# Kernel optimization log

Measured on AMD Instinct MI355X. Metric: run time of the kernel, lower is better.

Reference implementation:

```python
import jax, jax.numpy as jnp
import numpy as np

KS = 5          # kernel_size
D = 2           # spatial dim
DX = 0.01       # region kernel spacing
SCALE = 1.0
NX, NY = 32, 32
N = NX * NY


def _region_kernel():
    # gaussians.region_kernel: KS x KS grid of offsets spaced DX, centered at 0
    off = (jnp.arange(KS, dtype=jnp.float32) - (KS - 1) / 2.0) * DX
    gx, gy = jnp.meshgrid(off, off, indexing='ij')
    return jnp.stack([gx, gy], -1).reshape(-1, D)  # (KS*KS, 2)


def _build_cov(scaling, transform):
    # Cholesky-style parameterization: L lower-triangular with diag=scaling,
    # off-diag=transform; cov = L @ L^T (d=2 closed form)
    s0, s1 = scaling[:, 0], scaling[:, 1]
    t = transform[:, 0]
    c00 = s0 * s0
    c01 = s0 * t
    c11 = t * t + s1 * s1
    return jnp.stack([jnp.stack([c00, c01], -1), jnp.stack([c01, c11], -1)], -2)


def _inv2x2(c):
    det = c[:, 0, 0] * c[:, 1, 1] - c[:, 0, 1] * c[:, 1, 0]
    inv = jnp.stack([jnp.stack([c[:, 1, 1], -c[:, 0, 1]], -1),
                     jnp.stack([-c[:, 1, 0], c[:, 0, 0]], -1)], -2)
    return inv / det[:, None, None]


def setup_inputs() -> dict:
    key = jax.random.key(0)
    ks = jax.random.split(key, 20)
    # Gaussian state: grid means as in __init__
    tx = jnp.linspace(-1.0, 1.0, NX) * SCALE
    ty = jnp.linspace(-1.0, 1.0, NY) * SCALE
    gx, gy = jnp.meshgrid(tx, ty, indexing='ij')
    means = jnp.stack([gx, gy], -1).reshape(-1, D).astype(jnp.float32)
    u = 0.1 * jax.random.normal(ks[0], (N, 1), jnp.float32)
    scaling = jnp.exp(-4.5 + 0.2 * jax.random.normal(ks[1], (N, D), jnp.float32)) * SCALE
    transform = 0.002 * jax.random.normal(ks[2], (N, 1), jnp.float32)
    opacities = 2.0 + 0.1 * jax.random.normal(ks[3], (N,), jnp.float32)
    # network weights (4 heads share the first 3 layer shapes)
    convW = 0.05 * jax.random.normal(ks[4], (4, 50, 3, KS, KS), jnp.float32)
    convb = 0.01 * jax.random.normal(ks[5], (4, 50), jnp.float32)
    embW = 0.3 * jax.random.normal(ks[6], (4, 7, 30), jnp.float32)
    embb = 0.01 * jax.random.normal(ks[7], (4, 30), jnp.float32)
    l1W = 0.1 * jax.random.normal(ks[8], (4, 80, 80), jnp.float32)
    l1b = 0.01 * jax.random.normal(ks[9], (4, 80), jnp.float32)
    outW_sol = 0.1 * jax.random.normal(ks[10], (80, 1), jnp.float32)
    outb_sol = 0.01 * jax.random.normal(ks[11], (1,), jnp.float32)
    outW_trans = 0.1 * jax.random.normal(ks[12], (80, 2), jnp.float32)
    outb_trans = 0.01 * jax.random.normal(ks[13], (2,), jnp.float32)
    outW_scale = 0.1 * jax.random.normal(ks[14], (80, 2), jnp.float32)
    outb_scale = 0.01 * jax.random.normal(ks[15], (2,), jnp.float32)
    outW_tform = 0.1 * jax.random.normal(ks[16], (80, 1), jnp.float32)
    outb_tform = 0.01 * jax.random.normal(ks[17], (1,), jnp.float32)
    return {"means": means, "u": u, "scaling": scaling, "transform": transform,
            "opacities": opacities, "convW": convW, "convb": convb,
            "embW": embW, "embb": embb, "l1W": l1W, "l1b": l1b,
            "outW_sol": outW_sol, "outb_sol": outb_sol,
            "outW_trans": outW_trans, "outb_trans": outb_trans,
            "outW_scale": outW_scale, "outb_scale": outb_scale,
            "outW_tform": outW_tform, "outb_tform": outb_tform}


def reference(means, u, scaling, transform, opacities, convW, convb, embW, embb,
              l1W, l1b, outW_sol, outb_sol, outW_trans, outb_trans,
              outW_scale, outb_scale, outW_tform, outb_tform):
    n = means.shape[0]
    cov = _build_cov(scaling, transform)          # (N,2,2)
    conics = _inv2x2(cov)                         # (N,2,2)

    # --- sampling (torch.no_grad block in original) ---
    kern = _region_kernel()                                        # (25,2)
    samples = (means[:, None, :] + kern[None]).reshape(-1, D)      # (M,2), M=N*25
    bc = jnp.all(jnp.abs(samples) < SCALE, -1).astype(means.dtype)[:, None]
    alpha = jax.nn.sigmoid(opacities)                              # (N,)
    diff = samples[:, None, :] - means[None, :, :]                 # (M,N,2)
    Cq = jnp.einsum('nij,mnj->mni', conics, diff)                  # (M,N,2)
    G = jnp.exp(-0.5 * jnp.einsum('mni,mni->mn', diff, Cq)) * alpha[None, :]  # (M,N)
    u_s = G @ u                                                    # (M,1)
    # DIFFUSION pde_rhs = trace of laplacian: sum_n G * (|C q|^2 - tr(C)) * u_n
    trC = conics[:, 0, 0] + conics[:, 1, 1]
    lap = jnp.einsum('mn,mn,nc->mc', G, (Cq ** 2).sum(-1) - trC[None, :], u)  # (M,1)
    in_samples = jax.lax.stop_gradient(jnp.concatenate([u_s, lap, bc], -1))   # (M,3)

    # (N, 25, 3) -> (N, 3, 5, 5)
    img = in_samples.reshape(n, KS * KS, -1).transpose(0, 2, 1).reshape(n, -1, KS, KS)
    in_params = jnp.concatenate([means, u, scaling, transform, opacities[:, None]], -1)  # (N,7)

    # 4 Networks: conv(5x5 -> 1x1, 50ch) + param embed(7->30) + MLP(80->80->out)
    y = jnp.tanh(jnp.einsum('ncij,kocij->kno', img, convW) + convb[:, None, :])   # (4,N,50)
    e = jnp.tanh(jnp.einsum('nf,kfg->kng', in_params, embW) + embb[:, None, :])   # (4,N,30)
    h = jnp.tanh(jnp.einsum('knf,kfg->kng', jnp.concatenate([y, e], -1), l1W)
                 + l1b[:, None, :])                                               # (4,N,80)

    deltas = h[0] @ outW_sol + outb_sol          # (N,1)
    translation = h[1] @ outW_trans + outb_trans # (N,2)
    dscale = h[2] @ outW_scale + outb_scale      # (N,2)
    dtransform = h[3] @ outW_tform + outb_tform  # (N,1)

    u_new = u + deltas
    means_new = means + translation
    scaling_new = scaling * jnp.exp(dscale)
    transform_new = transform + dtransform
    cov_new = _build_cov(scaling_new, transform_new)
    return (u_new, means_new, scaling_new, transform_new, cov_new)
```

## Files before the change

### kernel.cpp

```cpp
#include <hip/hip_runtime.h>
#include <hip/hip_bf16.h>


#define NG 1024
#define GCAP 320

__device__ __forceinline__ float tanh_fast(float x) {
    return 1.0f - 2.0f / (__expf(2.0f * x) + 1.0f);
}

__global__ __launch_bounds__(256) void k_fused(
    const float* __restrict__ means, const float* __restrict__ u,
    const float* __restrict__ scal, const float* __restrict__ trans,
    const float* __restrict__ opac,
    const float* __restrict__ convW, const float* __restrict__ convb,
    const float* __restrict__ embW,  const float* __restrict__ embb,
    const float* __restrict__ l1W,   const float* __restrict__ l1b,
    const float* __restrict__ oWs,  const float* __restrict__ obs,
    const float* __restrict__ oWt,  const float* __restrict__ obt,
    const float* __restrict__ oWsc, const float* __restrict__ obsc,
    const float* __restrict__ oWtf, const float* __restrict__ obtf,
    float* __restrict__ out)
{
    __shared__ float gcomp[GCAP * 8];
    __shared__ float s1w[64 * 80];
    __shared__ float pus[2][2][32];
    __shared__ float plap[2][2][32];
    __shared__ float simg[2][80];
    __shared__ float hin[2][4][80];
    __shared__ float hv[2][4][80];
    __shared__ float semb[840];
    __shared__ float sembb[120];
    __shared__ float shead[480];
    __shared__ float sheadb[6];
    __shared__ int   cnt;

    const int t  = threadIdx.x;
    const int n0 = blockIdx.x * 2;

    const float mx0 = means[2*n0],   my0 = means[2*n0+1];
    const float mx1 = means[2*n0+2], my1 = means[2*n0+3];
    const float uu0 = u[n0],     uu1 = u[n0+1];
    const float sc00 = scal[2*n0],   sc01 = scal[2*n0+1];
    const float sc10 = scal[2*n0+2], sc11 = scal[2*n0+3];
    const float tr0 = trans[n0], tr1 = trans[n0+1];
    const float op0 = opac[n0],  op1 = opac[n0+1];

    float wcv[75];
    {
        const float* w = convW + (size_t)(t < 200 ? t : 0) * 75;
        #pragma unroll
        for (int j = 0; j < 75; ++j) wcv[j] = w[j];
    }
    float w1[80];
    {
        int k = t / 80, g = t - (t / 80) * 80;
        const float* w = l1W + (size_t)(k * 80) * 80 + g;
        #pragma unroll
        for (int f = 0; f < 80; ++f) w1[f] = w[f * 80];
    }
    float bcv  = (t < 200) ? convb[t] : 0.0f;
    float b1   = l1b[t];
    float b1k3 = l1b[256 + (t & 63)];

    for (int i = t; i < 5120; i += 256) {
        int f = i >> 6, g16 = i & 63;
        s1w[i] = l1W[(240 + f) * 80 + 16 + g16];
    }
    for (int i = t; i < 840; i += 256) semb[i] = embW[i];
    if (t < 120) sembb[t] = embb[t];
    for (int i = t; i < 480; i += 256) {
        float v = (i < 80) ? oWs[i] : (i < 240) ? oWt[i - 80]
                : (i < 400) ? oWsc[i - 240] : oWtf[i - 400];
        shead[i] = v;
    }
    if (t < 6) sheadb[t] = (t == 0) ? obs[0] : (t < 3) ? obt[t-1]
                         : (t < 5) ? obsc[t-3] : obtf[0];

    const float bxmin = fminf(mx0, mx1) - 0.02f, bxmax = fmaxf(mx0, mx1) + 0.02f;
    const float bymin = fminf(my0, my1) - 0.02f, bymax = fmaxf(my0, my1) + 0.02f;

    if (t == 0) cnt = 0;
    __syncthreads();
    for (int g = t; g < NG; g += 256) {
        float gmx = means[2*g], gmy = means[2*g+1];
        float s0  = scal[2*g],  s1  = scal[2*g+1];
        float tt  = trans[g];
        float c00 = s0*s0, c01 = s0*tt, c11 = tt*tt + s1*s1;
        float r2  = 100.0f * (c00 + c11);
        float ddx = fmaxf(fmaxf(bxmin - gmx, gmx - bxmax), 0.0f);
        float ddy = fmaxf(fmaxf(bymin - gmy, gmy - bymax), 0.0f);
        if (ddx*ddx + ddy*ddy <= r2) {
            float idet = 1.0f / (c00*c11 - c01*c01);
            float A = c11*idet, B = -c01*idet, C = c00*idet;
            float alpha = 1.0f / (1.0f + __expf(-opac[g]));
            int slot = atomicAdd(&cnt, 1);
            if (slot < GCAP) {
                float4* dst = (float4*)(gcomp + slot*8);
                dst[0] = make_float4(gmx, gmy, A, B);
                dst[1] = make_float4(C, A + C, alpha * u[g], 0.0f);
            }
        }
    }
    __syncthreads();
    const int nsurv = min(cnt, GCAP);

    {
        int w = t >> 6, lane = t & 63;
        int l = w >> 1;
        int hc = ((w & 1) << 1) | (lane >> 5);
        int s  = lane & 31; if (s > 24) s = 24;
        int si = s / 5, sj = s - si * 5;
        float gx = l ? mx1 : mx0, gy = l ? my1 : my0;
        float sx = gx + (float)(si - 2) * 0.01f;
        float sy = gy + (float)(sj - 2) * 0.01f;
        float us = 0.0f, lp = 0.0f;
        #pragma unroll 2
        for (int i = hc; i < nsurv; i += 4) {
            float4 a = *(const float4*)(gcomp + i*8);
            float4 b = *(const float4*)(gcomp + i*8 + 4);
            float dx = sx - a.x, dy = sy - a.y;
            float Cq0 = a.z*dx + a.w*dy;
            float Cq1 = a.w*dx + b.x*dy;
            float q   = dx*Cq0 + dy*Cq1;
            float e   = __expf(-0.5f*q) * b.z;
            us += e;
            lp += e * (Cq0*Cq0 + Cq1*Cq1 - b.y);
        }
        us += __shfl_down(us, 32);
        lp += __shfl_down(lp, 32);
        if ((lane & 31) == s && lane < 32) {
            pus[l][w & 1][s] = us; plap[l][w & 1][s] = lp;
        }
    }
    __syncthreads();

    if (t < 50) {
        int l = t / 25, s = t - l * 25;
        float us = pus[l][0][s] + pus[l][1][s];
        float lp = plap[l][0][s] + plap[l][1][s];
        int si = s / 5, sj = s - si * 5;
        float gx = l ? mx1 : mx0, gy = l ? my1 : my0;
        float sx = gx + (float)(si - 2) * 0.01f;
        float sy = gy + (float)(sj - 2) * 0.01f;
        simg[l][s]      = us;
        simg[l][25 + s] = lp;
        simg[l][50 + s] = (fabsf(sx) < 1.0f && fabsf(sy) < 1.0f) ? 1.0f : 0.0f;
    }
    __syncthreads();

    if (t < 200) {
        float a0 = bcv, a1 = bcv;
        #pragma unroll
        for (int j = 0; j < 75; ++j) {
            a0 += simg[0][j] * wcv[j];
            a1 += simg[1][j] * wcv[j];
        }
        int k = t / 50, o = t - k * 50;
        hin[0][k][o] = tanh_fast(a0);
        hin[1][k][o] = tanh_fast(a1);
    } else {
        for (int idx = t - 200; idx < 240; idx += 56) {
            int l = idx / 120, rem = idx - l * 120;
            int k = rem / 30, g = rem - k * 30;
            float acc = sembb[k * 30 + g];
            #pragma unroll
            for (int f = 0; f < 7; ++f) {
                float in0, in1;
                switch (f) {
                    case 0: in0 = mx0;  in1 = mx1;  break;
                    case 1: in0 = my0;  in1 = my1;  break;
                    case 2: in0 = uu0;  in1 = uu1;  break;
                    case 3: in0 = sc00; in1 = sc10; break;
                    case 4: in0 = sc01; in1 = sc11; break;
                    case 5: in0 = tr0;  in1 = tr1;  break;
                    default: in0 = op0; in1 = op1;  break;
                }
                acc += (l ? in1 : in0) * semb[(k*7 + f)*30 + g];
            }
            hin[l][k][50 + g] = tanh_fast(acc);
        }
    }
    __syncthreads();

    {
        int k = t / 80, g = t - (t / 80) * 80;
        float a0 = b1, a1 = b1;
        #pragma unroll
        for (int f = 0; f < 80; ++f) {
            a0 += hin[0][k][f] * w1[f];
            a1 += hin[1][k][f] * w1[f];
        }
        hv[0][k][g] = tanh_fast(a0);
        hv[1][k][g] = tanh_fast(a1);
    }
    if (t < 64) {
        int g = 16 + t;
        float a0 = b1k3, a1 = b1k3;
        #pragma unroll 8
        for (int f = 0; f < 80; ++f) {
            float w = s1w[(f << 6) | t];
            a0 += hin[0][3][f] * w;
            a1 += hin[1][3][f] * w;
        }
        hv[0][3][g] = tanh_fast(a0);
        hv[1][3][g] = tanh_fast(a1);
    }
    __syncthreads();

    if (t < 64) {
        int l = (t / 6) & 1, t6 = t % 6;
        int k, base, stride, j;
        if (t6 == 0)      { k = 0; base = 0;   stride = 1; j = 0; }
        else if (t6 < 3)  { k = 1; base = 80;  stride = 2; j = t6 - 1; }
        else if (t6 < 5)  { k = 2; base = 240; stride = 2; j = t6 - 3; }
        else              { k = 3; base = 400; stride = 1; j = 0; }
        float acc = sheadb[t6];
        #pragma unroll 8
        for (int f = 0; f < 80; ++f)
            acc += hv[l][k][f] * shead[base + f * stride + j];

        int sb = (t / 6) * 6;
        float o0 = __shfl(acc, sb + 0);
        float o1 = __shfl(acc, sb + 1);
        float o2 = __shfl(acc, sb + 2);
        float o3 = __shfl(acc, sb + 3);
        float o4 = __shfl(acc, sb + 4);
        float o5 = __shfl(acc, sb + 5);

        if (t == 0 || t == 6) {
            int n = n0 + (t / 6);
            float uu = t ? uu1 : uu0;
            float s0 = t ? sc10 : sc00, s1 = t ? sc11 : sc01;
            float tr = t ? tr1 : tr0;
            float u_new = uu + o0;
            float mxn = (t ? mx1 : mx0) + o1;
            float myn = (t ? my1 : my0) + o2;
            float s0n = s0 * __expf(o3);
            float s1n = s1 * __expf(o4);
            float tn  = tr + o5;
            float c00 = s0n*s0n, c01 = s0n*tn, c11 = tn*tn + s1n*s1n;
            out[n]              = u_new;
            out[1024 + 2*n]     = mxn;
            out[1024 + 2*n + 1] = myn;
            out[3072 + 2*n]     = s0n;
            out[3072 + 2*n + 1] = s1n;
            out[5120 + n]       = tn;
            out[6144 + 4*n]     = c00;
            out[6144 + 4*n + 1] = c01;
            out[6144 + 4*n + 2] = c01;
            out[6144 + 4*n + 3] = c11;
        }
    }
}

extern "C" void kernel_launch(void* const* d_in, const int* in_sizes, int n_in,
                              void* d_out, int out_size, void* d_ws, size_t ws_size,
                              hipStream_t stream)
{
    k_fused<<<dim3(NG / 2), dim3(256), 0, stream>>>(
        (const float*)d_in[0],  (const float*)d_in[1],  (const float*)d_in[2],
        (const float*)d_in[3],  (const float*)d_in[4],  (const float*)d_in[5],
        (const float*)d_in[6],  (const float*)d_in[7],  (const float*)d_in[8],
        (const float*)d_in[9],  (const float*)d_in[10], (const float*)d_in[11],
        (const float*)d_in[12], (const float*)d_in[13], (const float*)d_in[14],
        (const float*)d_in[15], (const float*)d_in[16], (const float*)d_in[17],
        (const float*)d_in[18], (float*)d_out);
}
```

Measured before the change: 105.4 us.

## Process eight Gaussians per block with 512 threads to amortize weight loads

Each block now handles eight Gaussians instead of two, with 512 threads and 128 blocks instead of 512. The per-block cost of loading conv and MLP weights into registers and of culling the neighbour list is shared across more Gaussians, and the dense layers accumulate eight outputs per thread. The trade-offs are fewer blocks on the device, a larger bounding box that lets more Gaussians survive culling (with GCAP overflow possible), and higher register pressure at 512 threads, where the wcv and w1 arrays could spill.

```diff
diff --git a/kernel.cpp b/kernel.cpp
--- a/kernel.cpp
+++ b/kernel.cpp
@@ -9,7 +9,7 @@
     return 1.0f - 2.0f / (__expf(2.0f * x) + 1.0f);
 }
 
-__global__ __launch_bounds__(256) void k_fused(
+__global__ __launch_bounds__(512) void k_fused(
     const float* __restrict__ means, const float* __restrict__ u,
     const float* __restrict__ scal, const float* __restrict__ trans,
     const float* __restrict__ opac,
@@ -23,12 +23,12 @@
     float* __restrict__ out)
 {
     __shared__ float gcomp[GCAP * 8];
-    __shared__ float s1w[64 * 80];
-    __shared__ float pus[2][2][32];
-    __shared__ float plap[2][2][32];
-    __shared__ float simg[2][80];
-    __shared__ float hin[2][4][80];
-    __shared__ float hv[2][4][80];
+    __shared__ float pus[8][32];
+    __shared__ float plap[8][32];
+    __shared__ float simg[8][80];
+    __shared__ float hin[8][4][80];
+    __shared__ float hv[8][4][80];
+    __shared__ float sin_[8][8];
     __shared__ float semb[840];
     __shared__ float sembb[120];
     __shared__ float shead[480];
@@ -36,15 +36,7 @@
     __shared__ int   cnt;
 
     const int t  = threadIdx.x;
-    const int n0 = blockIdx.x * 2;
-
-    const float mx0 = means[2*n0],   my0 = means[2*n0+1];
-    const float mx1 = means[2*n0+2], my1 = means[2*n0+3];
-    const float uu0 = u[n0],     uu1 = u[n0+1];
-    const float sc00 = scal[2*n0],   sc01 = scal[2*n0+1];
-    const float sc10 = scal[2*n0+2], sc11 = scal[2*n0+3];
-    const float tr0 = trans[n0], tr1 = trans[n0+1];
-    const float op0 = opac[n0],  op1 = opac[n0+1];
+    const int n0 = blockIdx.x * 8;
 
     float wcv[75];
     {
@@ -54,35 +46,47 @@
     }
     float w1[80];
     {
-        int k = t / 80, g = t - (t / 80) * 80;
+        int p = (t < 320) ? t : 0;
+        int k = p / 80, g = p - (p / 80) * 80;
         const float* w = l1W + (size_t)(k * 80) * 80 + g;
         #pragma unroll
         for (int f = 0; f < 80; ++f) w1[f] = w[f * 80];
     }
-    float bcv  = (t < 200) ? convb[t] : 0.0f;
-    float b1   = l1b[t];
-    float b1k3 = l1b[256 + (t & 63)];
-
-    for (int i = t; i < 5120; i += 256) {
-        int f = i >> 6, g16 = i & 63;
-        s1w[i] = l1W[(240 + f) * 80 + 16 + g16];
-    }
-    for (int i = t; i < 840; i += 256) semb[i] = embW[i];
+    float bcv = (t < 200) ? convb[t] : 0.0f;
+    float b1  = (t < 320) ? l1b[t]  : 0.0f;
+
+    for (int i = t; i < 840; i += 512) semb[i] = embW[i];
     if (t < 120) sembb[t] = embb[t];
-    for (int i = t; i < 480; i += 256) {
+    if (t >= 128 && t < 608 - 0) {
+    }
+    for (int i = t; i < 480; i += 512) {
         float v = (i < 80) ? oWs[i] : (i < 240) ? oWt[i - 80]
                 : (i < 400) ? oWsc[i - 240] : oWtf[i - 400];
         shead[i] = v;
     }
     if (t < 6) sheadb[t] = (t == 0) ? obs[0] : (t < 3) ? obt[t-1]
                          : (t < 5) ? obsc[t-3] : obtf[0];
-
-    const float bxmin = fminf(mx0, mx1) - 0.02f, bxmax = fmaxf(mx0, mx1) + 0.02f;
-    const float bymin = fminf(my0, my1) - 0.02f, bymax = fmaxf(my0, my1) + 0.02f;
+    if (t < 56) {
+        int g8 = t / 7, f = t - g8 * 7;
+        int n = n0 + g8;
+        float v = (f == 0) ? means[2*n] : (f == 1) ? means[2*n+1]
+                : (f == 2) ? u[n]       : (f == 3) ? scal[2*n]
+                : (f == 4) ? scal[2*n+1]: (f == 5) ? trans[n] : opac[n];
+        sin_[g8][f] = v;
+    }
+
+    float bxmin = 1e30f, bxmax = -1e30f, bymin = 1e30f, bymax = -1e30f;
+    #pragma unroll
+    for (int l = 0; l < 8; ++l) {
+        float gx = means[2*(n0 + l)], gy = means[2*(n0 + l) + 1];
+        bxmin = fminf(bxmin, gx); bxmax = fmaxf(bxmax, gx);
+        bymin = fminf(bymin, gy); bymax = fmaxf(bymax, gy);
+    }
+    bxmin -= 0.02f; bxmax += 0.02f; bymin -= 0.02f; bymax += 0.02f;
 
     if (t == 0) cnt = 0;
     __syncthreads();
-    for (int g = t; g < NG; g += 256) {
+    for (int g = t; g < NG; g += 512) {
         float gmx = means[2*g], gmy = means[2*g+1];
         float s0  = scal[2*g],  s1  = scal[2*g+1];
         float tt  = trans[g];
@@ -107,16 +111,15 @@
 
     {
         int w = t >> 6, lane = t & 63;
-        int l = w >> 1;
-        int hc = ((w & 1) << 1) | (lane >> 5);
-        int s  = lane & 31; if (s > 24) s = 24;
+        int half = lane >> 5;
+        int s = lane & 31; if (s > 24) s = 24;
         int si = s / 5, sj = s - si * 5;
-        float gx = l ? mx1 : mx0, gy = l ? my1 : my0;
+        float gx = sin_[w][0], gy = sin_[w][1];
         float sx = gx + (float)(si - 2) * 0.01f;
         float sy = gy + (float)(sj - 2) * 0.01f;
         float us = 0.0f, lp = 0.0f;
         #pragma unroll 2
-        for (int i = hc; i < nsurv; i += 4) {
+        for (int i = half; i < nsurv; i += 2) {
             float4 a = *(const float4*)(gcomp + i*8);
             float4 b = *(const float4*)(gcomp + i*8 + 4);
             float dx = sx - a.x, dy = sy - a.y;
@@ -129,87 +132,67 @@
         }
         us += __shfl_down(us, 32);
         lp += __shfl_down(lp, 32);
-        if ((lane & 31) == s && lane < 32) {
-            pus[l][w & 1][s] = us; plap[l][w & 1][s] = lp;
-        }
-    }
-    __syncthreads();
-
-    if (t < 50) {
+        if (lane < 32 && (lane & 31) == s) {
+            pus[w][s] = us; plap[w][s] = lp;
+        }
+    }
+    __syncthreads();
+
+    if (t < 200) {
         int l = t / 25, s = t - l * 25;
-        float us = pus[l][0][s] + pus[l][1][s];
-        float lp = plap[l][0][s] + plap[l][1][s];
         int si = s / 5, sj = s - si * 5;
-        float gx = l ? mx1 : mx0, gy = l ? my1 : my0;
-        float sx = gx + (float)(si - 2) * 0.01f;
-        float sy = gy + (float)(sj - 2) * 0.01f;
-        simg[l][s]      = us;
-        simg[l][25 + s] = lp;
+        float sx = sin_[l][0] + (float)(si - 2) * 0.01f;
+        float sy = sin_[l][1] + (float)(sj - 2) * 0.01f;
+        simg[l][s]      = pus[l][s];
+        simg[l][25 + s] = plap[l][s];
         simg[l][50 + s] = (fabsf(sx) < 1.0f && fabsf(sy) < 1.0f) ? 1.0f : 0.0f;
     }
     __syncthreads();
 
     if (t < 200) {
-        float a0 = bcv, a1 = bcv;
-        #pragma unroll
+        float a[8];
+        #pragma unroll
+        for (int l = 0; l < 8; ++l) a[l] = bcv;
+        #pragma unroll 3
         for (int j = 0; j < 75; ++j) {
-            a0 += simg[0][j] * wcv[j];
-            a1 += simg[1][j] * wcv[j];
+            float w = wcv[j];
+            #pragma unroll
+            for (int l = 0; l < 8; ++l) a[l] += simg[l][j] * w;
         }
         int k = t / 50, o = t - k * 50;
-        hin[0][k][o] = tanh_fast(a0);
-        hin[1][k][o] = tanh_fast(a1);
+        #pragma unroll
+        for (int l = 0; l < 8; ++l) hin[l][k][o] = tanh_fast(a[l]);
     } else {
-        for (int idx = t - 200; idx < 240; idx += 56) {
+        for (int idx = t - 200; idx < 960; idx += 312) {
             int l = idx / 120, rem = idx - l * 120;
             int k = rem / 30, g = rem - k * 30;
             float acc = sembb[k * 30 + g];
             #pragma unroll
-            for (int f = 0; f < 7; ++f) {
-                float in0, in1;
-                switch (f) {
-                    case 0: in0 = mx0;  in1 = mx1;  break;
-                    case 1: in0 = my0;  in1 = my1;  break;
-                    case 2: in0 = uu0;  in1 = uu1;  break;
-                    case 3: in0 = sc00; in1 = sc10; break;
-                    case 4: in0 = sc01; in1 = sc11; break;
-                    case 5: in0 = tr0;  in1 = tr1;  break;
-                    default: in0 = op0; in1 = op1;  break;
-                }
-                acc += (l ? in1 : in0) * semb[(k*7 + f)*30 + g];
-            }
+            for (int f = 0; f < 7; ++f)
+                acc += sin_[l][f] * semb[(k*7 + f)*30 + g];
             hin[l][k][50 + g] = tanh_fast(acc);
         }
     }
     __syncthreads();
 
-    {
-        int k = t / 80, g = t - (t / 80) * 80;
-        float a0 = b1, a1 = b1;
-        #pragma unroll
+    if (t < 320) {
+        int k = t / 80, g = t - k * 80;
+        float a[8];
+        #pragma unroll
+        for (int l = 0; l < 8; ++l) a[l] = b1;
+        #pragma unroll 4
         for (int f = 0; f < 80; ++f) {
-            a0 += hin[0][k][f] * w1[f];
-            a1 += hin[1][k][f] * w1[f];
-        }
-        hv[0][k][g] = tanh_fast(a0);
-        hv[1][k][g] = tanh_fast(a1);
-    }
-    if (t < 64) {
-        int g = 16 + t;
-        float a0 = b1k3, a1 = b1k3;
-        #pragma unroll 8
-        for (int f = 0; f < 80; ++f) {
-            float w = s1w[(f << 6) | t];
-            a0 += hin[0][3][f] * w;
-            a1 += hin[1][3][f] * w;
-        }
-        hv[0][3][g] = tanh_fast(a0);
-        hv[1][3][g] = tanh_fast(a1);
-    }
-    __syncthreads();
-
-    if (t < 64) {
-        int l = (t / 6) & 1, t6 = t % 6;
+            float w = w1[f];
+            #pragma unroll
+            for (int l = 0; l < 8; ++l) a[l] += hin[l][k][f] * w;
+        }
+        #pragma unroll
+        for (int l = 0; l < 8; ++l) hv[l][k][g] = tanh_fast(a[l]);
+    }
+    __syncthreads();
+
+    if (t < 48) {
+        int l = t / 6, t6 = t - l * 6;
         int k, base, stride, j;
         if (t6 == 0)      { k = 0; base = 0;   stride = 1; j = 0; }
         else if (t6 < 3)  { k = 1; base = 80;  stride = 2; j = t6 - 1; }
@@ -220,7 +203,7 @@
         for (int f = 0; f < 80; ++f)
             acc += hv[l][k][f] * shead[base + f * stride + j];
 
-        int sb = (t / 6) * 6;
+        int sb = l * 6;
         float o0 = __shfl(acc, sb + 0);
         float o1 = __shfl(acc, sb + 1);
         float o2 = __shfl(acc, sb + 2);
@@ -228,14 +211,14 @@
         float o4 = __shfl(acc, sb + 4);
         float o5 = __shfl(acc, sb + 5);
 
-        if (t == 0 || t == 6) {
-            int n = n0 + (t / 6);
-            float uu = t ? uu1 : uu0;
-            float s0 = t ? sc10 : sc00, s1 = t ? sc11 : sc01;
-            float tr = t ? tr1 : tr0;
+        if (t6 == 0) {
+            int n = n0 + l;
+            float uu = sin_[l][2];
+            float s0 = sin_[l][3], s1 = sin_[l][4];
+            float tr = sin_[l][5];
             float u_new = uu + o0;
-            float mxn = (t ? mx1 : mx0) + o1;
-            float myn = (t ? my1 : my0) + o2;
+            float mxn = sin_[l][0] + o1;
+            float myn = sin_[l][1] + o2;
             float s0n = s0 * __expf(o3);
             float s1n = s1 * __expf(o4);
             float tn  = tr + o5;
@@ -258,7 +241,7 @@
                               void* d_out, int out_size, void* d_ws, size_t ws_size,
                               hipStream_t stream)
 {
-    k_fused<<<dim3(NG / 2), dim3(256), 0, stream>>>(
+    k_fused<<<dim3(NG / 8), dim3(512), 0, stream>>>(
         (const float*)d_in[0],  (const float*)d_in[1],  (const float*)d_in[2],
         (const float*)d_in[3],  (const float*)d_in[4],  (const float*)d_in[5],
         (const float*)d_in[6],  (const float*)d_in[7],  (const float*)d_in[8],
```

After: 127.8 us. +21.2%, slower.
